# Performance work log

Hardware: AMD Instinct MI355X
Metric: run time of the kernel (lower is better)

The kernel has to match this reference:

```python
import jax, jax.numpy as jnp
import numpy as np

EPS = 1e-6

def rmsnorm(x, w):
    # x: (B, N, D), w: (D,)
    var = jnp.mean(jnp.square(x), axis=-1, keepdims=True)
    return x * jax.lax.rsqrt(var + EPS) * w

def head_mixing(x):
    # Parameter-free cross-head mix: split each head's D dims into N chunks
    # and transpose the (head, chunk) axes. x: (B, N, D), D % N == 0.
    B, N, D = x.shape
    c = D // N
    return x.reshape(B, N, N, c).transpose(0, 2, 1, 3).reshape(B, N, D)

def setup_inputs() -> dict:
    key = jax.random.key(0)
    ks = jax.random.split(key, 4)
    B, N, D, H = 8192, 16, 256, 512
    return {
        "x": jax.random.normal(ks[0], (B, N, D), dtype=jnp.float32),
        "norm1_w": jnp.ones((D,), dtype=jnp.float32),
        "norm2_w": jnp.ones((D,), dtype=jnp.float32),
        "w1": jax.random.normal(ks[1], (N, D, H), dtype=jnp.float32) * (1.0 / np.sqrt(D)),
        "w3": jax.random.normal(ks[2], (N, D, H), dtype=jnp.float32) * (1.0 / np.sqrt(D)),
        "w2": jax.random.normal(ks[3], (N, H, D), dtype=jnp.float32) * (1.0 / np.sqrt(H)),
    }

def reference(x, norm1_w, norm2_w, w1, w3, w2):
    # P = HeadMixing(RMSNorm(X)) + X
    p = head_mixing(rmsnorm(x, norm1_w)) + x
    # Q = PerHeadSwiGLUFFN(RMSNorm(P)) + P  (grouped per-head SwiGLU)
    pn = rmsnorm(p, norm2_w)                       # (B, N, D)
    g = jnp.einsum('bnd,ndh->bnh', pn, w1)         # gate proj
    u = jnp.einsum('bnd,ndh->bnh', pn, w3)         # up proj
    h = jax.nn.silu(g) * u                         # (B, N, H)
    q = jnp.einsum('bnh,nhd->bnd', h, w2) + p
    return q
```

## Files before the change

### kernel.cpp

```cpp
#include <hip/hip_runtime.h>
#include <hip/hip_bf16.h>

#define B_ 8192
#define N_ 16
#define D_ 256
#define H_ 512

using bf16x8 = __attribute__((ext_vector_type(8))) short;
using f32x4  = __attribute__((ext_vector_type(4))) float;

__device__ __forceinline__ void gload_lds16(const void* g, void* l) {
    __builtin_amdgcn_global_load_lds(
        (const __attribute__((address_space(1))) void*)g,
        (__attribute__((address_space(3))) void*)l, 16, 0, 0);
}

__device__ __forceinline__ short f2bf(float f) {
    unsigned int u = __float_as_uint(f);
    u += 0x7fffu + ((u >> 16) & 1u);
    return (short)(u >> 16);
}

__device__ __forceinline__ float bf2f(short s) {
    return __uint_as_float(((unsigned int)(unsigned short)s) << 16);
}

__device__ __forceinline__ f32x4 mfma(bf16x8 a, bf16x8 b, f32x4 c) {
    return __builtin_amdgcn_mfma_f32_16x16x32_bf16(a, b, c, 0, 0, 0);
}

__device__ __forceinline__ void stage_ab(const short* __restrict__ Ag, int sA,
                                         const short* __restrict__ Bg, int sB,
                                         int k0, short* Al, short* Bl, int t) {
#pragma unroll
    for (int rnd = 0; rnd < 4; ++rnd) {
        int flat = rnd * 512 + t;
        int row = flat >> 3, g = flat & 7;
        int sg = (g ^ row) & 7;
        gload_lds16(Ag + (size_t)row * sA + k0 + sg * 8, Al + flat * 8);
    }
#pragma unroll
    for (int rnd = 0; rnd < 4; ++rnd) {
        int flat = rnd * 512 + t;
        int row = flat >> 3, g = flat & 7;
        int sg = (g ^ row) & 7;
        gload_lds16(Bg + (size_t)row * sB + k0 + sg * 8, Bl + flat * 8);
    }
}

__device__ __forceinline__ bf16x8 rdfrag(const short* base, int row, int g) {
    int gp = (g ^ row) & 7;
    return *(const bf16x8*)&base[(row << 6) + (gp << 3)];
}

template<int NT>
__device__ __forceinline__ void gemm_core(const short* __restrict__ Ag, int sA,
                                          const short* __restrict__ Bg, int sB,
                                          short* lds, f32x4 (&acc)[8][4],
                                          int t, int rowA0, int rowB0) {
    int lane = t & 63;
    int l16 = lane & 15, kq = lane >> 4;

    stage_ab(Ag, sA, Bg, sB, 0, lds, lds + 32768, t);
    __syncthreads();

#pragma unroll 1
    for (int kt = 0; kt < NT; ++kt) {
        short* Asl = lds + (kt & 1) * 16384;
        short* Bsl = lds + 32768 + (kt & 1) * 16384;
        if (kt + 1 < NT)
            stage_ab(Ag, sA, Bg, sB, (kt + 1) * 64,
                     lds + ((kt + 1) & 1) * 16384,
                     lds + 32768 + ((kt + 1) & 1) * 16384, t);

        bf16x8 aF[4], bF[4];
#pragma unroll
        for (int j = 0; j < 4; ++j)
            bF[j] = rdfrag(Bsl, rowB0 + j * 16 + l16, kq);
#pragma unroll
        for (int i = 0; i < 4; ++i)
            aF[i] = rdfrag(Asl, rowA0 + i * 16 + l16, kq);
#pragma unroll
        for (int i = 0; i < 4; ++i)
#pragma unroll
            for (int j = 0; j < 4; ++j)
                acc[i][j] = mfma(aF[i], bF[j], acc[i][j]);
#pragma unroll
        for (int i = 0; i < 4; ++i)
            aF[i] = rdfrag(Asl, rowA0 + 64 + i * 16 + l16, kq);
#pragma unroll
        for (int i = 0; i < 4; ++i)
#pragma unroll
            for (int j = 0; j < 4; ++j)
                acc[4 + i][j] = mfma(aF[i], bF[j], acc[4 + i][j]);
#pragma unroll
        for (int j = 0; j < 4; ++j)
            bF[j] = rdfrag(Bsl, rowB0 + j * 16 + l16, 4 + kq);
#pragma unroll
        for (int i = 0; i < 4; ++i)
            aF[i] = rdfrag(Asl, rowA0 + i * 16 + l16, 4 + kq);
#pragma unroll
        for (int i = 0; i < 4; ++i)
#pragma unroll
            for (int j = 0; j < 4; ++j)
                acc[i][j] = mfma(aF[i], bF[j], acc[i][j]);
#pragma unroll
        for (int i = 0; i < 4; ++i)
            aF[i] = rdfrag(Asl, rowA0 + 64 + i * 16 + l16, 4 + kq);
#pragma unroll
        for (int i = 0; i < 4; ++i)
#pragma unroll
            for (int j = 0; j < 4; ++j)
                acc[4 + i][j] = mfma(aF[i], bF[j], acc[4 + i][j]);

        __syncthreads();
    }
}

__global__ __launch_bounds__(256) void k_prep(const float* __restrict__ w1,
                                              const float* __restrict__ w3,
                                              const float* __restrict__ w2,
                                              short* __restrict__ wgu,
                                              short* __restrict__ w2t) {
    int o = blockIdx.x * 256 + threadIdx.x;
    int n = o >> 17;
    int r = o & 131071;
    int h = r >> 8, d = r & 255;
    size_t base = ((size_t)n * 1024 + (h >> 4) * 32 + (h & 15)) * 256 + d;
    wgu[base]            = f2bf(w1[(size_t)n * 131072 + (size_t)d * 512 + h]);
    wgu[base + 16 * 256] = f2bf(w3[(size_t)n * 131072 + (size_t)d * 512 + h]);
    int d2 = r >> 9, h2 = r & 511;
    w2t[o] = f2bf(w2[(size_t)n * 131072 + (size_t)h2 * 256 + d2]);
}

__global__ __launch_bounds__(256) void k_mix(const float* __restrict__ x,
                                             const float* __restrict__ n1w,
                                             const float* __restrict__ n2w,
                                             short* __restrict__ pb_ws,
                                             short* __restrict__ pn_ws) {
    __shared__ float xs[N_ * D_];
    __shared__ float ps[N_ * D_];
    __shared__ float inv1[N_];
    __shared__ float inv2[N_];
    int b = blockIdx.x;
    int t = threadIdx.x;

    const float4* xb4 = (const float4*)(x + (size_t)b * (N_ * D_));
    float4* xs4 = (float4*)xs;
#pragma unroll
    for (int i = 0; i < 4; ++i) xs4[t + i * 256] = xb4[t + i * 256];
    __syncthreads();

    int hh = t >> 4, sub = t & 15;
    float s = 0.f;
#pragma unroll
    for (int j = 0; j < 16; ++j) { float v = xs[hh * 256 + sub * 16 + j]; s += v * v; }
    s += __shfl_xor(s, 1); s += __shfl_xor(s, 2);
    s += __shfl_xor(s, 4); s += __shfl_xor(s, 8);
    if (sub == 0) inv1[hh] = rsqrtf(s * (1.0f / 256.0f) + 1e-6f);
    __syncthreads();

    {
        int n = t >> 4, j = t & 15;
#pragma unroll 1
        for (int m = 0; m < 16; ++m) {
            float v = xs[n * 256 + m * 16 + j] * inv1[n] * n1w[m * 16 + j]
                    + xs[m * 256 + t];
            ps[m * 256 + t] = v;
        }
    }
    __syncthreads();

    float s2 = 0.f;
#pragma unroll
    for (int j = 0; j < 16; ++j) { float v = ps[hh * 256 + sub * 16 + j]; s2 += v * v; }
    s2 += __shfl_xor(s2, 1); s2 += __shfl_xor(s2, 2);
    s2 += __shfl_xor(s2, 4); s2 += __shfl_xor(s2, 8);
    if (sub == 0) inv2[hh] = rsqrtf(s2 * (1.0f / 256.0f) + 1e-6f);
    __syncthreads();

#pragma unroll 1
    for (int m = 0; m < 16; ++m) {
        float v = ps[m * 256 + t];
        size_t off = ((size_t)m * B_ + b) * D_ + t;
        pb_ws[off] = f2bf(v);
        pn_ws[off] = f2bf(v * inv2[m] * n2w[t]);
    }
}

__global__ __launch_bounds__(512, 2) void k_gu(const short* __restrict__ pn,
                                               const short* __restrict__ wgu,
                                               short* __restrict__ hact) {
    extern __shared__ char smem[];
    short* lds = (short*)smem;

    int bid = blockIdx.x;
    int bx = (bid & 7) * 256 + (bid >> 3);
    int head = bx >> 7;
    int mt = (bx >> 2) & 31;
    int nt = bx & 3;

    int t = threadIdx.x;
    int w = t >> 6, lane = t & 63;
    int l16 = lane & 15, kq = lane >> 4;
    int wm = w >> 2, wn = w & 3;

    f32x4 acc[8][4];
#pragma unroll
    for (int i = 0; i < 8; ++i)
#pragma unroll
        for (int j = 0; j < 4; ++j) acc[i][j] = (f32x4){0.f, 0.f, 0.f, 0.f};

    const short* Ag = pn  + ((size_t)head * B_ + (size_t)mt * 256) * D_;
    const short* Bg = wgu + ((size_t)head * 1024 + (size_t)nt * 256) * D_;

    gemm_core<4>(Ag, D_, Bg, D_, lds, acc, t, wm * 128, wn * 64);

    size_t hb = (size_t)head * B_ * H_;
#pragma unroll
    for (int mf = 0; mf < 8; ++mf) {
        int m = mt * 256 + wm * 128 + mf * 16 + kq * 4;
#pragma unroll
        for (int p = 0; p < 2; ++p) {
            int h = (nt * 8 + wn * 2 + p) * 16 + l16;
#pragma unroll
            for (int r = 0; r < 4; ++r) {
                float g = acc[mf][2 * p][r];
                float u = acc[mf][2 * p + 1][r];
                float hv = g * (1.0f / (1.0f + __expf(-g))) * u;
                hact[hb + (size_t)(m + r) * H_ + h] = f2bf(hv);
            }
        }
    }
}

__global__ __launch_bounds__(512, 2) void k_dn(const short* __restrict__ hact,
                                               const short* __restrict__ w2t,
                                               const short* __restrict__ pb,
                                               float* __restrict__ out) {
    extern __shared__ char smem[];
    short* lds = (short*)smem;

    int bid = blockIdx.x;
    int bx = (bid & 7) * 64 + (bid >> 3);
    int head = bx >> 5;
    int mt = bx & 31;

    int t = threadIdx.x;
    int w = t >> 6, lane = t & 63;
    int l16 = lane & 15, kq = lane >> 4;
    int wm = w >> 2, wn = w & 3;

    f32x4 acc[8][4];
#pragma unroll
    for (int i = 0; i < 8; ++i)
#pragma unroll
        for (int j = 0; j < 4; ++j) acc[i][j] = (f32x4){0.f, 0.f, 0.f, 0.f};

    const short* Ag = hact + ((size_t)head * B_ + (size_t)mt * 256) * H_;
    const short* Bg = w2t  + (size_t)head * D_ * H_;

    gemm_core<8>(Ag, H_, Bg, H_, lds, acc, t, wm * 128, wn * 64);

#pragma unroll
    for (int mf = 0; mf < 8; ++mf) {
        int m = mt * 256 + wm * 128 + mf * 16 + kq * 4;
#pragma unroll
        for (int nf = 0; nf < 4; ++nf) {
            int d = wn * 64 + nf * 16 + l16;
#pragma unroll
            for (int r = 0; r < 4; ++r) {
                float v = acc[mf][nf][r]
                        + bf2f(pb[((size_t)head * B_ + m + r) * D_ + d]);
                out[(size_t)(m + r) * (N_ * D_) + head * D_ + d] = v;
            }
        }
    }
}

extern "C" void kernel_launch(void* const* d_in, const int* in_sizes, int n_in,
                              void* d_out, int out_size, void* d_ws, size_t ws_size,
                              hipStream_t stream) {
    const float* x   = (const float*)d_in[0];
    const float* n1w = (const float*)d_in[1];
    const float* n2w = (const float*)d_in[2];
    const float* w1  = (const float*)d_in[3];
    const float* w3  = (const float*)d_in[4];
    const float* w2  = (const float*)d_in[5];
    float* out = (float*)d_out;

    char* ws = (char*)d_ws;
    short* wgu  = (short*)(ws);
    short* w2t  = (short*)(ws + (8ull   << 20));
    short* pn   = (short*)(ws + (12ull  << 20));
    short* pb   = (short*)(ws + (76ull  << 20));
    short* hact = (short*)(ws + (140ull << 20));

    (void)hipFuncSetAttribute((const void*)k_gu,
                              hipFuncAttributeMaxDynamicSharedMemorySize, 131072);
    (void)hipFuncSetAttribute((const void*)k_dn,
                              hipFuncAttributeMaxDynamicSharedMemorySize, 131072);

    k_prep<<<(N_ * D_ * H_) / 256, 256, 0, stream>>>(w1, w3, w2, wgu, w2t);
    k_mix<<<B_, 256, 0, stream>>>(x, n1w, n2w, pb, pn);
    k_gu<<<N_ * (B_ / 256) * 4, 512, 131072, stream>>>(pn, wgu, hact);
    k_dn<<<N_ * (B_ / 256), 512, 131072, stream>>>(hact, w2t, pb, out);
}
```

Before: 296.7 us.

## Shrink GEMM tiles to 128x128 with small single-buffered LDS and vectorize mix stores

Replaces the 256x256-tile, 512-thread, double-buffered 128KB-LDS GEMM core with a 128x128 tile, 256-thread, K=32 single-buffered core using 16KB of static LDS, targeting higher occupancy (4 blocks per CU) and more blocks. The mix kernel now computes row norms with float4 loads and full-wave reductions, and writes packed bf16 pairs as 32-bit stores. The GEMM tradeoff is that global-to-LDS loads are no longer overlapped with MFMA inside a block, and each tile has lower arithmetic intensity, so the kernel relies on co-resident blocks to hide latency.

```diff
diff --git a/kernel.cpp b/kernel.cpp
--- a/kernel.cpp
+++ b/kernel.cpp
@@ -25,94 +25,60 @@
     return __uint_as_float(((unsigned int)(unsigned short)s) << 16);
 }
 
+__device__ __forceinline__ unsigned int pack2(float lo, float hi) {
+    return (unsigned int)(unsigned short)f2bf(lo)
+         | ((unsigned int)(unsigned short)f2bf(hi) << 16);
+}
+
 __device__ __forceinline__ f32x4 mfma(bf16x8 a, bf16x8 b, f32x4 c) {
     return __builtin_amdgcn_mfma_f32_16x16x32_bf16(a, b, c, 0, 0, 0);
 }
 
-__device__ __forceinline__ void stage_ab(const short* __restrict__ Ag, int sA,
-                                         const short* __restrict__ Bg, int sB,
-                                         int k0, short* Al, short* Bl, int t) {
-#pragma unroll
-    for (int rnd = 0; rnd < 4; ++rnd) {
-        int flat = rnd * 512 + t;
-        int row = flat >> 3, g = flat & 7;
-        int sg = (g ^ row) & 7;
-        gload_lds16(Ag + (size_t)row * sA + k0 + sg * 8, Al + flat * 8);
-    }
-#pragma unroll
-    for (int rnd = 0; rnd < 4; ++rnd) {
-        int flat = rnd * 512 + t;
-        int row = flat >> 3, g = flat & 7;
-        int sg = (g ^ row) & 7;
-        gload_lds16(Bg + (size_t)row * sB + k0 + sg * 8, Bl + flat * 8);
-    }
-}
-
-__device__ __forceinline__ bf16x8 rdfrag(const short* base, int row, int g) {
-    int gp = (g ^ row) & 7;
-    return *(const bf16x8*)&base[(row << 6) + (gp << 3)];
+__device__ __forceinline__ bf16x8 rd32(const short* base, int row, int g) {
+    int gp = (g ^ row) & 3;
+    return *(const bf16x8*)&base[(row << 5) + (gp << 3)];
 }
 
 template<int NT>
-__device__ __forceinline__ void gemm_core(const short* __restrict__ Ag, int sA,
-                                          const short* __restrict__ Bg, int sB,
-                                          short* lds, f32x4 (&acc)[8][4],
-                                          int t, int rowA0, int rowB0) {
+__device__ __forceinline__ void gemm97(const short* __restrict__ Ag, int sA,
+                                       const short* __restrict__ Bg, int sB,
+                                       short* As, short* Bs,
+                                       f32x4 (&acc)[4][4],
+                                       int t, int rowA0, int rowB0) {
     int lane = t & 63;
     int l16 = lane & 15, kq = lane >> 4;
 
-    stage_ab(Ag, sA, Bg, sB, 0, lds, lds + 32768, t);
-    __syncthreads();
-
 #pragma unroll 1
     for (int kt = 0; kt < NT; ++kt) {
-        short* Asl = lds + (kt & 1) * 16384;
-        short* Bsl = lds + 32768 + (kt & 1) * 16384;
-        if (kt + 1 < NT)
-            stage_ab(Ag, sA, Bg, sB, (kt + 1) * 64,
-                     lds + ((kt + 1) & 1) * 16384,
-                     lds + 32768 + ((kt + 1) & 1) * 16384, t);
+        int k0 = kt * 32;
+#pragma unroll
+        for (int rnd = 0; rnd < 2; ++rnd) {
+            int flat = rnd * 256 + t;
+            int row = flat >> 2, g = flat & 3;
+            int sg = (g ^ row) & 3;
+            gload_lds16(Ag + (size_t)row * sA + k0 + sg * 8, As + flat * 8);
+        }
+#pragma unroll
+        for (int rnd = 0; rnd < 2; ++rnd) {
+            int flat = rnd * 256 + t;
+            int row = flat >> 2, g = flat & 3;
+            int sg = (g ^ row) & 3;
+            gload_lds16(Bg + (size_t)row * sB + k0 + sg * 8, Bs + flat * 8);
+        }
+        __syncthreads();
 
         bf16x8 aF[4], bF[4];
 #pragma unroll
         for (int j = 0; j < 4; ++j)
-            bF[j] = rdfrag(Bsl, rowB0 + j * 16 + l16, kq);
+            bF[j] = rd32(Bs, rowB0 + j * 16 + l16, kq);
 #pragma unroll
         for (int i = 0; i < 4; ++i)
-            aF[i] = rdfrag(Asl, rowA0 + i * 16 + l16, kq);
+            aF[i] = rd32(As, rowA0 + i * 16 + l16, kq);
 #pragma unroll
         for (int i = 0; i < 4; ++i)
 #pragma unroll
             for (int j = 0; j < 4; ++j)
                 acc[i][j] = mfma(aF[i], bF[j], acc[i][j]);
-#pragma unroll
-        for (int i = 0; i < 4; ++i)
-            aF[i] = rdfrag(Asl, rowA0 + 64 + i * 16 + l16, kq);
-#pragma unroll
-        for (int i = 0; i < 4; ++i)
-#pragma unroll
-            for (int j = 0; j < 4; ++j)
-                acc[4 + i][j] = mfma(aF[i], bF[j], acc[4 + i][j]);
-#pragma unroll
-        for (int j = 0; j < 4; ++j)
-            bF[j] = rdfrag(Bsl, rowB0 + j * 16 + l16, 4 + kq);
-#pragma unroll
-        for (int i = 0; i < 4; ++i)
-            aF[i] = rdfrag(Asl, rowA0 + i * 16 + l16, 4 + kq);
-#pragma unroll
-        for (int i = 0; i < 4; ++i)
-#pragma unroll
-            for (int j = 0; j < 4; ++j)
-                acc[i][j] = mfma(aF[i], bF[j], acc[i][j]);
-#pragma unroll
-        for (int i = 0; i < 4; ++i)
-            aF[i] = rdfrag(Asl, rowA0 + 64 + i * 16 + l16, 4 + kq);
-#pragma unroll
-        for (int i = 0; i < 4; ++i)
-#pragma unroll
-            for (int j = 0; j < 4; ++j)
-                acc[4 + i][j] = mfma(aF[i], bF[j], acc[4 + i][j]);
-
         __syncthreads();
     }
 }
@@ -136,93 +102,107 @@
 __global__ __launch_bounds__(256) void k_mix(const float* __restrict__ x,
                                              const float* __restrict__ n1w,
                                              const float* __restrict__ n2w,
-                                             short* __restrict__ pb_ws,
-                                             short* __restrict__ pn_ws) {
-    __shared__ float xs[N_ * D_];
-    __shared__ float ps[N_ * D_];
+                                             unsigned int* __restrict__ pb_u,
+                                             unsigned int* __restrict__ pn_u) {
+    __shared__ __align__(16) float xs[N_ * D_];
+    __shared__ __align__(16) float ps[N_ * D_];
     __shared__ float inv1[N_];
     __shared__ float inv2[N_];
     int b = blockIdx.x;
     int t = threadIdx.x;
+    int w = t >> 6, lane = t & 63;
 
     const float4* xb4 = (const float4*)(x + (size_t)b * (N_ * D_));
     float4* xs4 = (float4*)xs;
+    float4* ps4 = (float4*)ps;
 #pragma unroll
     for (int i = 0; i < 4; ++i) xs4[t + i * 256] = xb4[t + i * 256];
     __syncthreads();
 
-    int hh = t >> 4, sub = t & 15;
-    float s = 0.f;
-#pragma unroll
-    for (int j = 0; j < 16; ++j) { float v = xs[hh * 256 + sub * 16 + j]; s += v * v; }
-    s += __shfl_xor(s, 1); s += __shfl_xor(s, 2);
-    s += __shfl_xor(s, 4); s += __shfl_xor(s, 8);
-    if (sub == 0) inv1[hh] = rsqrtf(s * (1.0f / 256.0f) + 1e-6f);
+#pragma unroll
+    for (int q = 0; q < 4; ++q) {
+        int row = w * 4 + q;
+        float4 v = xs4[row * 64 + lane];
+        float s = v.x * v.x + v.y * v.y + v.z * v.z + v.w * v.w;
+        s += __shfl_xor(s, 1);  s += __shfl_xor(s, 2);
+        s += __shfl_xor(s, 4);  s += __shfl_xor(s, 8);
+        s += __shfl_xor(s, 16); s += __shfl_xor(s, 32);
+        if (lane == 0) inv1[row] = rsqrtf(s * (1.0f / 256.0f) + 1e-6f);
+    }
     __syncthreads();
 
     {
         int n = t >> 4, j = t & 15;
+        float i1 = inv1[n];
 #pragma unroll 1
         for (int m = 0; m < 16; ++m) {
-            float v = xs[n * 256 + m * 16 + j] * inv1[n] * n1w[m * 16 + j]
+            float v = xs[n * 256 + m * 16 + j] * i1 * n1w[m * 16 + j]
                     + xs[m * 256 + t];
             ps[m * 256 + t] = v;
         }
     }
     __syncthreads();
 
-    float s2 = 0.f;
-#pragma unroll
-    for (int j = 0; j < 16; ++j) { float v = ps[hh * 256 + sub * 16 + j]; s2 += v * v; }
-    s2 += __shfl_xor(s2, 1); s2 += __shfl_xor(s2, 2);
-    s2 += __shfl_xor(s2, 4); s2 += __shfl_xor(s2, 8);
-    if (sub == 0) inv2[hh] = rsqrtf(s2 * (1.0f / 256.0f) + 1e-6f);
-    __syncthreads();
-
-#pragma unroll 1
-    for (int m = 0; m < 16; ++m) {
-        float v = ps[m * 256 + t];
-        size_t off = ((size_t)m * B_ + b) * D_ + t;
-        pb_ws[off] = f2bf(v);
-        pn_ws[off] = f2bf(v * inv2[m] * n2w[t]);
-    }
-}
-
-__global__ __launch_bounds__(512, 2) void k_gu(const short* __restrict__ pn,
+#pragma unroll
+    for (int q = 0; q < 4; ++q) {
+        int row = w * 4 + q;
+        float4 v = ps4[row * 64 + lane];
+        float s = v.x * v.x + v.y * v.y + v.z * v.z + v.w * v.w;
+        s += __shfl_xor(s, 1);  s += __shfl_xor(s, 2);
+        s += __shfl_xor(s, 4);  s += __shfl_xor(s, 8);
+        s += __shfl_xor(s, 16); s += __shfl_xor(s, 32);
+        if (lane == 0) inv2[row] = rsqrtf(s * (1.0f / 256.0f) + 1e-6f);
+    }
+    __syncthreads();
+
+    int dh = t & 127, mh = t >> 7;
+    float wA = n2w[2 * dh], wB = n2w[2 * dh + 1];
+#pragma unroll
+    for (int i = 0; i < 8; ++i) {
+        int m = mh * 8 + i;
+        float2 f = *(const float2*)&ps[m * 256 + 2 * dh];
+        float iv = inv2[m];
+        size_t off = ((size_t)m * B_ + b) * (D_ / 2) + dh;
+        pb_u[off] = pack2(f.x, f.y);
+        pn_u[off] = pack2(f.x * iv * wA, f.y * iv * wB);
+    }
+}
+
+__global__ __launch_bounds__(256, 4) void k_gu(const short* __restrict__ pn,
                                                const short* __restrict__ wgu,
                                                short* __restrict__ hact) {
-    extern __shared__ char smem[];
-    short* lds = (short*)smem;
+    __shared__ __align__(16) short As[128 * 32];
+    __shared__ __align__(16) short Bs[128 * 32];
 
     int bid = blockIdx.x;
-    int bx = (bid & 7) * 256 + (bid >> 3);
-    int head = bx >> 7;
-    int mt = (bx >> 2) & 31;
-    int nt = bx & 3;
+    int bx = (bid & 7) * 1024 + (bid >> 3);
+    int head = bx >> 9;
+    int mt = (bx >> 3) & 63;
+    int nt = bx & 7;
 
     int t = threadIdx.x;
     int w = t >> 6, lane = t & 63;
     int l16 = lane & 15, kq = lane >> 4;
-    int wm = w >> 2, wn = w & 3;
-
-    f32x4 acc[8][4];
-#pragma unroll
-    for (int i = 0; i < 8; ++i)
+    int wm = w >> 1, wn = w & 1;
+
+    f32x4 acc[4][4];
+#pragma unroll
+    for (int i = 0; i < 4; ++i)
 #pragma unroll
         for (int j = 0; j < 4; ++j) acc[i][j] = (f32x4){0.f, 0.f, 0.f, 0.f};
 
-    const short* Ag = pn  + ((size_t)head * B_ + (size_t)mt * 256) * D_;
-    const short* Bg = wgu + ((size_t)head * 1024 + (size_t)nt * 256) * D_;
-
-    gemm_core<4>(Ag, D_, Bg, D_, lds, acc, t, wm * 128, wn * 64);
+    const short* Ag = pn  + ((size_t)head * B_ + (size_t)mt * 128) * D_;
+    const short* Bg = wgu + ((size_t)head * 1024 + (size_t)nt * 128) * D_;
+
+    gemm97<8>(Ag, D_, Bg, D_, As, Bs, acc, t, wm * 64, wn * 64);
 
     size_t hb = (size_t)head * B_ * H_;
 #pragma unroll
-    for (int mf = 0; mf < 8; ++mf) {
-        int m = mt * 256 + wm * 128 + mf * 16 + kq * 4;
+    for (int mf = 0; mf < 4; ++mf) {
+        int m = mt * 128 + wm * 64 + mf * 16 + kq * 4;
 #pragma unroll
         for (int p = 0; p < 2; ++p) {
-            int h = (nt * 8 + wn * 2 + p) * 16 + l16;
+            int h = nt * 64 + (wn * 2 + p) * 16 + l16;
 #pragma unroll
             for (int r = 0; r < 4; ++r) {
                 float g = acc[mf][2 * p][r];
@@ -234,40 +214,41 @@
     }
 }
 
-__global__ __launch_bounds__(512, 2) void k_dn(const short* __restrict__ hact,
+__global__ __launch_bounds__(256, 4) void k_dn(const short* __restrict__ hact,
                                                const short* __restrict__ w2t,
                                                const short* __restrict__ pb,
                                                float* __restrict__ out) {
-    extern __shared__ char smem[];
-    short* lds = (short*)smem;
+    __shared__ __align__(16) short As[128 * 32];
+    __shared__ __align__(16) short Bs[128 * 32];
 
     int bid = blockIdx.x;
-    int bx = (bid & 7) * 64 + (bid >> 3);
-    int head = bx >> 5;
-    int mt = bx & 31;
+    int bx = (bid & 7) * 256 + (bid >> 3);
+    int head = bx >> 7;
+    int mt = (bx >> 1) & 63;
+    int nt = bx & 1;
 
     int t = threadIdx.x;
     int w = t >> 6, lane = t & 63;
     int l16 = lane & 15, kq = lane >> 4;
-    int wm = w >> 2, wn = w & 3;
-
-    f32x4 acc[8][4];
-#pragma unroll
-    for (int i = 0; i < 8; ++i)
+    int wm = w >> 1, wn = w & 1;
+
+    f32x4 acc[4][4];
+#pragma unroll
+    for (int i = 0; i < 4; ++i)
 #pragma unroll
         for (int j = 0; j < 4; ++j) acc[i][j] = (f32x4){0.f, 0.f, 0.f, 0.f};
 
-    const short* Ag = hact + ((size_t)head * B_ + (size_t)mt * 256) * H_;
-    const short* Bg = w2t  + (size_t)head * D_ * H_;
-
-    gemm_core<8>(Ag, H_, Bg, H_, lds, acc, t, wm * 128, wn * 64);
-
-#pragma unroll
-    for (int mf = 0; mf < 8; ++mf) {
-        int m = mt * 256 + wm * 128 + mf * 16 + kq * 4;
+    const short* Ag = hact + ((size_t)head * B_ + (size_t)mt * 128) * H_;
+    const short* Bg = w2t  + ((size_t)head * D_ + (size_t)nt * 128) * H_;
+
+    gemm97<16>(Ag, H_, Bg, H_, As, Bs, acc, t, wm * 64, wn * 64);
+
+#pragma unroll
+    for (int mf = 0; mf < 4; ++mf) {
+        int m = mt * 128 + wm * 64 + mf * 16 + kq * 4;
 #pragma unroll
         for (int nf = 0; nf < 4; ++nf) {
-            int d = wn * 64 + nf * 16 + l16;
+            int d = nt * 128 + wn * 64 + nf * 16 + l16;
 #pragma unroll
             for (int r = 0; r < 4; ++r) {
                 float v = acc[mf][nf][r]
@@ -296,13 +277,9 @@
     short* pb   = (short*)(ws + (76ull  << 20));
     short* hact = (short*)(ws + (140ull << 20));
 
-    (void)hipFuncSetAttribute((const void*)k_gu,
-                              hipFuncAttributeMaxDynamicSharedMemorySize, 131072);
-    (void)hipFuncSetAttribute((const void*)k_dn,
-                              hipFuncAttributeMaxDynamicSharedMemorySize, 131072);
-
     k_prep<<<(N_ * D_ * H_) / 256, 256, 0, stream>>>(w1, w3, w2, wgu, w2t);
-    k_mix<<<B_, 256, 0, stream>>>(x, n1w, n2w, pb, pn);
-    k_gu<<<N_ * (B_ / 256) * 4, 512, 131072, stream>>>(pn, wgu, hact);
-    k_dn<<<N_ * (B_ / 256), 512, 131072, stream>>>(hact, w2t, pb, out);
-}
+    k_mix<<<B_, 256, 0, stream>>>(x, n1w, n2w,
+                                  (unsigned int*)pb, (unsigned int*)pn);
+    k_gu<<<N_ * (B_ / 128) * (1024 / 128), 256, 0, stream>>>(pn, wgu, hact);
+    k_dn<<<N_ * (B_ / 128) * (D_ / 128), 256, 0, stream>>>(hact, w2t, pb, out);
+}
```

Result: no change. 296.5 us (-0.0%).
